# Kernel optimization log

Measured on AMD Instinct MI355X. Metric: run time of the kernel, lower is better.

The kernel has to match this reference:

```python
import jax, jax.numpy as jnp
import numpy as np

N = 100000
IN_C = 256
OUT_C = 256
E = 500000


def gcn_conv(x, W, b, edges):
    """PyG GCNConv: add self-loops, symmetric D^-1/2 (A+I) D^-1/2 normalization,
    then scatter-add of transformed source features into targets, plus bias."""
    n = x.shape[0]
    loop = jnp.arange(n, dtype=edges.dtype)
    row = jnp.concatenate([edges[0], loop])  # source
    col = jnp.concatenate([edges[1], loop])  # target
    deg = jax.ops.segment_sum(jnp.ones_like(col, dtype=x.dtype), col, num_segments=n)
    dis = jax.lax.rsqrt(deg)  # deg >= 1 after self-loops
    norm = dis[row] * dis[col]  # [E+n]
    h = x @ W  # [n, out]
    msg = h[row] * norm[:, None]  # gather + scale
    return jax.ops.segment_sum(msg, col, num_segments=n) + b


def setup_inputs() -> dict:
    key = jax.random.key(0)
    ks = jax.random.split(key, 24)
    x = jax.random.normal(ks[0], (N, IN_C), dtype=jnp.float32)
    edges00 = jax.random.randint(ks[1], (2, E), 0, N, dtype=jnp.int32)
    edges01 = jax.random.randint(ks[2], (2, E), 0, N, dtype=jnp.int32)
    edges10 = jax.random.randint(ks[3], (2, E), 0, N, dtype=jnp.int32)
    edges11 = jax.random.randint(ks[4], (2, E), 0, N, dtype=jnp.int32)
    t0 = (jax.random.uniform(ks[5], (N,)) > 0.5).astype(jnp.float32)
    t1 = 1.0 - t0
    scale = 1.0 / np.sqrt(IN_C)
    W1 = jax.random.normal(ks[6], (IN_C, OUT_C), dtype=jnp.float32) * scale
    W2 = jax.random.normal(ks[7], (IN_C, OUT_C), dtype=jnp.float32) * scale
    W3 = jax.random.normal(ks[8], (IN_C, OUT_C), dtype=jnp.float32) * scale
    W4 = jax.random.normal(ks[9], (IN_C, OUT_C), dtype=jnp.float32) * scale
    b1 = jnp.zeros((OUT_C,), jnp.float32)
    b2 = jnp.zeros((OUT_C,), jnp.float32)
    b3 = jnp.zeros((OUT_C,), jnp.float32)
    b4 = jnp.zeros((OUT_C,), jnp.float32)
    p0 = jax.random.normal(ks[10], (OUT_C,), dtype=jnp.float32)
    p1 = jax.random.normal(ks[11], (OUT_C,), dtype=jnp.float32)
    p2 = jax.random.normal(ks[12], (OUT_C,), dtype=jnp.float32)
    p3 = jax.random.normal(ks[13], (OUT_C,), dtype=jnp.float32)
    p4 = jax.random.normal(ks[14], (OUT_C,), dtype=jnp.float32)
    p5 = jax.random.normal(ks[15], (OUT_C,), dtype=jnp.float32)
    return dict(x=x, edges00=edges00, edges01=edges01, edges10=edges10, edges11=edges11,
                type0_idx=t0, type1_idx=t1,
                W1=W1, b1=b1, W2=W2, b2=b2, W3=W3, b3=b3, W4=W4, b4=b4,
                p0=p0, p1=p1, p2=p2, p3=p3, p4=p4, p5=p5)


def reference(x, edges00, edges01, edges10, edges11, type0_idx, type1_idx,
              W1, b1, W2, b2, W3, b3, W4, b4, p0, p1, p2, p3, p4, p5):
    # x0/x1: first feature column masked by node type, broadcast over out channels
    x0c = type0_idx * x[:, 0]  # [N]
    x1c = type1_idx * x[:, 0]
    x00 = gcn_conv(x, W1, b1, edges00)
    x01 = gcn_conv(x, W2, b2, edges01)
    x10 = gcn_conv(x, W3, b3, edges10)
    x11 = gcn_conv(x, W4, b4, edges11)
    out = (x0c[:, None] * p0 + x1c[:, None] * p1
           + x00 * p2 + x01 * p3 + x10 * p4 + x11 * p5)
    return out
```

## Files before the change

kernel.cpp:

```cpp
#include <hip/hip_runtime.h>


typedef __bf16 v8bf __attribute__((ext_vector_type(8)));
typedef float v4f __attribute__((ext_vector_type(4)));

__device__ __forceinline__ unsigned short f2bf(float f) {
  unsigned u = __float_as_uint(f);
  u += 0x7fffu + ((u >> 16) & 1u);
  return (unsigned short)(u >> 16);
}
__device__ __forceinline__ float bf2f(unsigned short s) {
  return __uint_as_float(((unsigned)s) << 16);
}
__device__ __forceinline__ void async_ld16(const void* g, void* l) {
  __builtin_amdgcn_global_load_lds((__attribute__((address_space(1))) void*)g,
                                   (__attribute__((address_space(3))) void*)l,
                                   16, 0, 0);
}

__global__ void lc_zero(int* __restrict__ p, int n) {
  int i = blockIdx.x * 256 + threadIdx.x;
  if (i < n) p[i] = 0;
}

__global__ void lc_hist(const int* __restrict__ e0, const int* __restrict__ e1,
                        const int* __restrict__ e2, const int* __restrict__ e3,
                        int* __restrict__ hist, int N, int E) {
  int e = blockIdx.x * 256 + threadIdx.x;
  if (e >= E) return;
  int k = blockIdx.y;
  const int* ed = (k == 0) ? e0 : (k == 1) ? e1 : (k == 2) ? e2 : e3;
  int col = ed[E + e];
  atomicAdd(&hist[k * N + col], 1);
}

__global__ void lc_dis(const int* __restrict__ hist, float* __restrict__ dis, int M) {
  int i = blockIdx.x * 256 + threadIdx.x;
  if (i < M) dis[i] = rsqrtf((float)(hist[i] + 1));
}

__global__ void lc_scan1(const int* __restrict__ in, int* __restrict__ outp,
                         int* __restrict__ bsum, int M) {
  __shared__ int tmp[256];
  int t = threadIdx.x, i = blockIdx.x * 256 + t;
  int v = (i < M) ? in[i] : 0;
  tmp[t] = v;
  __syncthreads();
  for (int off = 1; off < 256; off <<= 1) {
    int add = (t >= off) ? tmp[t - off] : 0;
    __syncthreads();
    tmp[t] += add;
    __syncthreads();
  }
  if (i < M) outp[i] = tmp[t] - v;
  if (t == 255) bsum[blockIdx.x] = tmp[255];
}

__global__ void lc_scan2(int* __restrict__ bsum, int nb) {
  __shared__ int tmp[256];
  __shared__ int carry_s;
  int t = threadIdx.x;
  if (t == 0) carry_s = 0;
  __syncthreads();
  for (int base = 0; base < nb; base += 256) {
    int i = base + t;
    int v = (i < nb) ? bsum[i] : 0;
    tmp[t] = v;
    __syncthreads();
    for (int off = 1; off < 256; off <<= 1) {
      int add = (t >= off) ? tmp[t - off] : 0;
      __syncthreads();
      tmp[t] += add;
      __syncthreads();
    }
    int carry = carry_s;
    int total = tmp[255];
    if (i < nb) bsum[i] = carry + tmp[t] - v;
    __syncthreads();
    if (t == 0) carry_s = carry + total;
    __syncthreads();
  }
}

__global__ void lc_scan3(int* __restrict__ rp, int* __restrict__ cursor,
                         const int* __restrict__ bsum, int M) {
  int i = blockIdx.x * 256 + threadIdx.x;
  if (i < M) {
    int v = rp[i] + bsum[blockIdx.x];
    rp[i] = v;
    cursor[i] = v;
  }
}

__global__ void lc_fill(const int* __restrict__ e0, const int* __restrict__ e1,
                        const int* __restrict__ e2, const int* __restrict__ e3,
                        int* __restrict__ cursor, const float* __restrict__ dis,
                        int2* __restrict__ payload, int N, int E) {
  int e = blockIdx.x * 256 + threadIdx.x;
  if (e >= E) return;
  int k = blockIdx.y;
  const int* ed = (k == 0) ? e0 : (k == 1) ? e1 : (k == 2) ? e2 : e3;
  int src = ed[e], col = ed[E + e];
  int pos = atomicAdd(&cursor[k * N + col], 1);
  float nrm = dis[k * N + src] * dis[k * N + col];
  payload[pos] = make_int2(src, __float_as_int(nrm));
}

__global__ void lc_bias(const float* __restrict__ b1, const float* __restrict__ b2,
                        const float* __restrict__ b3, const float* __restrict__ b4,
                        const float* __restrict__ p2, const float* __restrict__ p3,
                        const float* __restrict__ p4, const float* __restrict__ p5,
                        float* __restrict__ biasc) {
  int c = threadIdx.x;
  biasc[c] = b1[c] * p2[c] + b2[c] * p3[c] + b3[c] * p4[c] + b4[c] * p5[c];
}

__global__ void lc_prep(const float* __restrict__ W1, const float* __restrict__ W2,
                        const float* __restrict__ W3, const float* __restrict__ W4,
                        const float* __restrict__ p2, const float* __restrict__ p3,
                        const float* __restrict__ p4, const float* __restrict__ p5,
                        unsigned short* __restrict__ Wt) {
  int b = blockIdx.x;
  int k = b >> 8, co = b & 255;
  int kk = threadIdx.x;
  const float* W = (k == 0) ? W1 : (k == 1) ? W2 : (k == 2) ? W3 : W4;
  const float* p = (k == 0) ? p2 : (k == 1) ? p3 : (k == 2) ? p4 : p5;
  Wt[(size_t)co * 1024 + k * 256 + kk] = f2bf(W[kk * 256 + co] * p[co]);
}

__global__ void lc_cvt(const float4* __restrict__ x4, ushort4* __restrict__ xb4,
                       const float* __restrict__ t0, const float* __restrict__ t1,
                       float* __restrict__ m0, float* __restrict__ m1, int n4) {
  int i = blockIdx.x * 256 + threadIdx.x;
  if (i >= n4) return;
  float4 v = x4[i];
  ushort4 r;
  r.x = f2bf(v.x); r.y = f2bf(v.y); r.z = f2bf(v.z); r.w = f2bf(v.w);
  xb4[i] = r;
  if ((i & 63) == 0) {
    int n = i >> 6;
    float xc = v.x;
    m0[n] = t0[n] * xc;
    m1[n] = t1[n] * xc;
  }
}

__global__ __launch_bounds__(256) void lc_aggx(
    const unsigned short* __restrict__ xb, unsigned short* __restrict__ Agg,
    int aggw, int kcount, int kbase, const int* __restrict__ rp,
    const int* __restrict__ hist, const float* __restrict__ dis,
    const int2* __restrict__ payload, int N) {
  int t = threadIdx.x;
  int w = t >> 6, lane = t & 63;
  int n, k, koff;
  if (kcount == 4) { n = blockIdx.x; k = w; koff = k * 256; }
  else { n = blockIdx.x * 4 + w; k = kbase; koff = 0; }
  if (n >= N) return;
  int c = lane * 4;
  int idx = k * N + n;

  float dn = dis[idx];
  float s = dn * dn;
  ushort4 hv = *(const ushort4*)&xb[(size_t)n * 256 + c];
  float a0 = bf2f(hv.x) * s, a1 = bf2f(hv.y) * s;
  float a2 = bf2f(hv.z) * s, a3 = bf2f(hv.w) * s;

  int start = rp[idx];
  int cnt = hist[idx];
  int i = 0;
  for (; i + 4 <= cnt; i += 4) {
    int2 e0 = payload[start + i];
    int2 e1 = payload[start + i + 1];
    int2 e2 = payload[start + i + 2];
    int2 e3 = payload[start + i + 3];
    ushort4 g0 = *(const ushort4*)&xb[(size_t)e0.x * 256 + c];
    ushort4 g1 = *(const ushort4*)&xb[(size_t)e1.x * 256 + c];
    ushort4 g2 = *(const ushort4*)&xb[(size_t)e2.x * 256 + c];
    ushort4 g3 = *(const ushort4*)&xb[(size_t)e3.x * 256 + c];
    float n0 = __int_as_float(e0.y), n1 = __int_as_float(e1.y);
    float n2 = __int_as_float(e2.y), n3 = __int_as_float(e3.y);
    a0 += bf2f(g0.x) * n0 + bf2f(g1.x) * n1 + bf2f(g2.x) * n2 + bf2f(g3.x) * n3;
    a1 += bf2f(g0.y) * n0 + bf2f(g1.y) * n1 + bf2f(g2.y) * n2 + bf2f(g3.y) * n3;
    a2 += bf2f(g0.z) * n0 + bf2f(g1.z) * n1 + bf2f(g2.z) * n2 + bf2f(g3.z) * n3;
    a3 += bf2f(g0.w) * n0 + bf2f(g1.w) * n1 + bf2f(g2.w) * n2 + bf2f(g3.w) * n3;
  }
  for (; i < cnt; i++) {
    int2 e0 = payload[start + i];
    ushort4 g0 = *(const ushort4*)&xb[(size_t)e0.x * 256 + c];
    float n0 = __int_as_float(e0.y);
    a0 += bf2f(g0.x) * n0;
    a1 += bf2f(g0.y) * n0;
    a2 += bf2f(g0.z) * n0;
    a3 += bf2f(g0.w) * n0;
  }
  ushort4 r;
  r.x = f2bf(a0); r.y = f2bf(a1); r.z = f2bf(a2); r.w = f2bf(a3);
  *(ushort4*)&Agg[(size_t)n * aggw + koff + c] = r;
}

__global__ __launch_bounds__(256) void lc_gemm(
    const unsigned short* __restrict__ A, int strideA,
    const unsigned short* __restrict__ B, int strideB, int K,
    float* __restrict__ out, int Mrows, int addprev, int doepi,
    const float* __restrict__ m0, const float* __restrict__ m1,
    const float* __restrict__ p0, const float* __restrict__ p1,
    const float* __restrict__ biasc) {
  __shared__ alignas(16) unsigned short As[128 * 32];
  __shared__ alignas(16) unsigned short Bs[128 * 32];
  int t = threadIdx.x;
  int w = t >> 6, lane = t & 63;
  int wm = w & 1, wn = w >> 1;
  int quad = lane >> 4, l16 = lane & 15;
  int row0 = blockIdx.x * 128, col0 = blockIdx.y * 128;

  v4f acc[4][4];
#pragma unroll
  for (int mt = 0; mt < 4; mt++)
#pragma unroll
    for (int nt = 0; nt < 4; nt++) {
      v4f z = {0.f, 0.f, 0.f, 0.f};
      acc[mt][nt] = z;
    }

  for (int kk = 0; kk < K; kk += 32) {
#pragma unroll
    for (int p = 0; p < 2; p++) {
      int cbase = p * 256 + w * 64;
      int cA = cbase + lane;
      int rl = cA >> 2, c16 = cA & 3;
      int grow = row0 + rl;
      if (grow >= Mrows) grow = Mrows - 1;
      async_ld16(A + (size_t)grow * strideA + kk + c16 * 8, &As[cbase * 8]);
      async_ld16(B + (size_t)(col0 + rl) * strideB + kk + c16 * 8, &Bs[cbase * 8]);
    }
    __syncthreads();

    v8bf af[4], bfr[4];
#pragma unroll
    for (int mt = 0; mt < 4; mt++) {
      int r = wm * 64 + mt * 16 + l16;
      af[mt] = *(const v8bf*)&As[r * 32 + quad * 8];
    }
#pragma unroll
    for (int nt = 0; nt < 4; nt++) {
      int n = wn * 64 + nt * 16 + l16;
      bfr[nt] = *(const v8bf*)&Bs[n * 32 + quad * 8];
    }
#pragma unroll
    for (int mt = 0; mt < 4; mt++)
#pragma unroll
      for (int nt = 0; nt < 4; nt++)
        acc[mt][nt] =
            __builtin_amdgcn_mfma_f32_16x16x32_bf16(af[mt], bfr[nt], acc[mt][nt], 0, 0, 0);
    __syncthreads();
  }

  float pc0[4], pc1[4], bc[4];
#pragma unroll
  for (int nt = 0; nt < 4; nt++) {
    int gcol = col0 + wn * 64 + nt * 16 + l16;
    pc0[nt] = doepi ? p0[gcol] : 0.f;
    pc1[nt] = doepi ? p1[gcol] : 0.f;
    bc[nt] = doepi ? biasc[gcol] : 0.f;
  }
#pragma unroll
  for (int mt = 0; mt < 4; mt++)
#pragma unroll
    for (int r = 0; r < 4; r++) {
      int grow = row0 + wm * 64 + mt * 16 + quad * 4 + r;
      if (grow >= Mrows) continue;
      float m0v = 0.f, m1v = 0.f;
      if (doepi) { m0v = m0[grow]; m1v = m1[grow]; }
#pragma unroll
      for (int nt = 0; nt < 4; nt++) {
        int gcol = col0 + wn * 64 + nt * 16 + l16;
        size_t o = (size_t)grow * 256 + gcol;
        float v = acc[mt][nt][r];
        if (addprev) v += out[o];
        if (doepi) v += m0v * pc0[nt] + m1v * pc1[nt] + bc[nt];
        out[o] = v;
      }
    }
}

extern "C" void kernel_launch(void* const* d_in, const int* in_sizes, int n_in,
                              void* d_out, int out_size, void* d_ws, size_t ws_size,
                              hipStream_t stream) {
  const float* x = (const float*)d_in[0];
  const int* e00 = (const int*)d_in[1];
  const int* e01 = (const int*)d_in[2];
  const int* e10 = (const int*)d_in[3];
  const int* e11 = (const int*)d_in[4];
  const float* t0 = (const float*)d_in[5];
  const float* t1 = (const float*)d_in[6];
  const float* W1 = (const float*)d_in[7];
  const float* b1 = (const float*)d_in[8];
  const float* W2 = (const float*)d_in[9];
  const float* b2 = (const float*)d_in[10];
  const float* W3 = (const float*)d_in[11];
  const float* b3 = (const float*)d_in[12];
  const float* W4 = (const float*)d_in[13];
  const float* b4 = (const float*)d_in[14];
  const float* p0 = (const float*)d_in[15];
  const float* p1 = (const float*)d_in[16];
  const float* p2 = (const float*)d_in[17];
  const float* p3 = (const float*)d_in[18];
  const float* p4 = (const float*)d_in[19];
  const float* p5 = (const float*)d_in[20];
  float* out = (float*)d_out;

  int N = in_sizes[0] / 256;
  int E = in_sizes[1] / 2;
  int M4 = 4 * N;
  int nb = (M4 + 255) / 256;

  char* wp = (char*)d_ws;
  auto carve = [&](size_t bytes) {
    void* r = (void*)wp;
    wp += (bytes + 255) & ~(size_t)255;
    return r;
  };
  unsigned short* xb = (unsigned short*)carve((size_t)N * 256 * 2);
  unsigned short* Wt = (unsigned short*)carve((size_t)256 * 1024 * 2);
  int* hist = (int*)carve((size_t)M4 * 4);
  float* dis = (float*)carve((size_t)M4 * 4);
  int* rp = (int*)carve((size_t)M4 * 4);
  int* cursor = (int*)carve((size_t)M4 * 4);
  int* bsum = (int*)carve((size_t)nb * 4);
  float* biasc = (float*)carve(256 * 4);
  float* m0 = (float*)carve((size_t)N * 4);
  float* m1 = (float*)carve((size_t)N * 4);
  int2* payload = (int2*)carve((size_t)4 * E * 8);
  size_t used = (size_t)(wp - (char*)d_ws);
  size_t remain = (ws_size > used) ? ws_size - used : 0;
  bool fat = remain >= (size_t)N * 1024 * 2;
  unsigned short* Agg = (unsigned short*)wp;

  int gE = (E + 255) / 256;
  int gM = (M4 + 255) / 256;

  lc_zero<<<gM, 256, 0, stream>>>(hist, M4);
  lc_hist<<<dim3(gE, 4), 256, 0, stream>>>(e00, e01, e10, e11, hist, N, E);
  lc_dis<<<gM, 256, 0, stream>>>(hist, dis, M4);
  lc_scan1<<<nb, 256, 0, stream>>>(hist, rp, bsum, M4);
  lc_scan2<<<1, 256, 0, stream>>>(bsum, nb);
  lc_scan3<<<nb, 256, 0, stream>>>(rp, cursor, bsum, M4);
  lc_fill<<<dim3(gE, 4), 256, 0, stream>>>(e00, e01, e10, e11, cursor, dis, payload, N, E);
  lc_bias<<<1, 256, 0, stream>>>(b1, b2, b3, b4, p2, p3, p4, p5, biasc);
  lc_prep<<<1024, 256, 0, stream>>>(W1, W2, W3, W4, p2, p3, p4, p5, Wt);
  lc_cvt<<<(N * 64 + 255) / 256, 256, 0, stream>>>((const float4*)x, (ushort4*)xb,
                                                   t0, t1, m0, m1, N * 64);

  int gemm_mb = (N + 127) / 128;
  if (fat) {
    lc_aggx<<<N, 256, 0, stream>>>(xb, Agg, 1024, 4, 0, rp, hist, dis, payload, N);
    lc_gemm<<<dim3(gemm_mb, 2), 256, 0, stream>>>(Agg, 1024, Wt, 1024, 1024, out, N,
                                                  0, 1, m0, m1, p0, p1, biasc);
  } else {
    for (int k = 0; k < 4; k++) {
      lc_aggx<<<(N + 3) / 4, 256, 0, stream>>>(xb, Agg, 256, 1, k, rp, hist, dis,
                                               payload, N);
      lc_gemm<<<dim3(gemm_mb, 2), 256, 0, stream>>>(Agg, 256, Wt + k * 256, 1024, 256,
                                                    out, N, (k > 0) ? 1 : 0,
                                                    (k == 3) ? 1 : 0, m0, m1, p0, p1,
                                                    biasc);
    }
  }
}
```

Baseline: 721.5 us.

## Fuse neighbor aggregation and GEMM into one kernel with aggregated rows kept in LDS

Replaces the separate aggregation kernel, which wrote a bf16 Agg buffer to global memory, and the tiled GEMM with one fused kernel. Each 512-thread block aggregates 32 nodes across all four edge types into a swizzled LDS tile, then runs MFMA directly against W read from global memory, and applies the epilogue. Two edge types are gathered at once per wave to raise memory-level parallelism. This removes the round trip of the intermediate through HBM and the extra launches. The trade-offs are 64KB of LDS per block and B operands read from global or cache with no LDS staging.

```diff
diff --git a/kernel.cpp b/kernel.cpp
--- a/kernel.cpp
+++ b/kernel.cpp
@@ -11,11 +11,6 @@
 }
 __device__ __forceinline__ float bf2f(unsigned short s) {
   return __uint_as_float(((unsigned)s) << 16);
-}
-__device__ __forceinline__ void async_ld16(const void* g, void* l) {
-  __builtin_amdgcn_global_load_lds((__attribute__((address_space(1))) void*)g,
-                                   (__attribute__((address_space(3))) void*)l,
-                                   16, 0, 0);
 }
 
 __global__ void lc_zero(int* __restrict__ p, int n) {
@@ -145,140 +140,128 @@
   }
 }
 
-__global__ __launch_bounds__(256) void lc_aggx(
-    const unsigned short* __restrict__ xb, unsigned short* __restrict__ Agg,
-    int aggw, int kcount, int kbase, const int* __restrict__ rp,
-    const int* __restrict__ hist, const float* __restrict__ dis,
-    const int2* __restrict__ payload, int N) {
-  int t = threadIdx.x;
-  int w = t >> 6, lane = t & 63;
-  int n, k, koff;
-  if (kcount == 4) { n = blockIdx.x; k = w; koff = k * 256; }
-  else { n = blockIdx.x * 4 + w; k = kbase; koff = 0; }
-  if (n >= N) return;
-  int c = lane * 4;
-  int idx = k * N + n;
-
-  float dn = dis[idx];
-  float s = dn * dn;
-  ushort4 hv = *(const ushort4*)&xb[(size_t)n * 256 + c];
-  float a0 = bf2f(hv.x) * s, a1 = bf2f(hv.y) * s;
-  float a2 = bf2f(hv.z) * s, a3 = bf2f(hv.w) * s;
-
-  int start = rp[idx];
-  int cnt = hist[idx];
-  int i = 0;
-  for (; i + 4 <= cnt; i += 4) {
-    int2 e0 = payload[start + i];
-    int2 e1 = payload[start + i + 1];
-    int2 e2 = payload[start + i + 2];
-    int2 e3 = payload[start + i + 3];
-    ushort4 g0 = *(const ushort4*)&xb[(size_t)e0.x * 256 + c];
-    ushort4 g1 = *(const ushort4*)&xb[(size_t)e1.x * 256 + c];
-    ushort4 g2 = *(const ushort4*)&xb[(size_t)e2.x * 256 + c];
-    ushort4 g3 = *(const ushort4*)&xb[(size_t)e3.x * 256 + c];
-    float n0 = __int_as_float(e0.y), n1 = __int_as_float(e1.y);
-    float n2 = __int_as_float(e2.y), n3 = __int_as_float(e3.y);
-    a0 += bf2f(g0.x) * n0 + bf2f(g1.x) * n1 + bf2f(g2.x) * n2 + bf2f(g3.x) * n3;
-    a1 += bf2f(g0.y) * n0 + bf2f(g1.y) * n1 + bf2f(g2.y) * n2 + bf2f(g3.y) * n3;
-    a2 += bf2f(g0.z) * n0 + bf2f(g1.z) * n1 + bf2f(g2.z) * n2 + bf2f(g3.z) * n3;
-    a3 += bf2f(g0.w) * n0 + bf2f(g1.w) * n1 + bf2f(g2.w) * n2 + bf2f(g3.w) * n3;
-  }
-  for (; i < cnt; i++) {
-    int2 e0 = payload[start + i];
-    ushort4 g0 = *(const ushort4*)&xb[(size_t)e0.x * 256 + c];
-    float n0 = __int_as_float(e0.y);
-    a0 += bf2f(g0.x) * n0;
-    a1 += bf2f(g0.y) * n0;
-    a2 += bf2f(g0.z) * n0;
-    a3 += bf2f(g0.w) * n0;
-  }
-  ushort4 r;
-  r.x = f2bf(a0); r.y = f2bf(a1); r.z = f2bf(a2); r.w = f2bf(a3);
-  *(ushort4*)&Agg[(size_t)n * aggw + koff + c] = r;
-}
-
-__global__ __launch_bounds__(256) void lc_gemm(
-    const unsigned short* __restrict__ A, int strideA,
-    const unsigned short* __restrict__ B, int strideB, int K,
-    float* __restrict__ out, int Mrows, int addprev, int doepi,
+#define GAT1(POS, A0, A1, A2, A3)                                       \
+  do {                                                                  \
+    int2 ee = payload[POS];                                             \
+    ushort4 gg = *(const ushort4*)&xb[(size_t)ee.x * 256 + c];          \
+    float nn = __int_as_float(ee.y);                                    \
+    A0 += bf2f(gg.x) * nn;                                              \
+    A1 += bf2f(gg.y) * nn;                                              \
+    A2 += bf2f(gg.z) * nn;                                              \
+    A3 += bf2f(gg.w) * nn;                                              \
+  } while (0)
+
+__global__ __launch_bounds__(512, 4) void lc_fused(
+    const unsigned short* __restrict__ xb, const unsigned short* __restrict__ Wt,
+    const int* __restrict__ rp, const int* __restrict__ hist,
+    const float* __restrict__ dis, const int2* __restrict__ payload,
+    float* __restrict__ out, int N,
     const float* __restrict__ m0, const float* __restrict__ m1,
     const float* __restrict__ p0, const float* __restrict__ p1,
     const float* __restrict__ biasc) {
-  __shared__ alignas(16) unsigned short As[128 * 32];
-  __shared__ alignas(16) unsigned short Bs[128 * 32];
-  int t = threadIdx.x;
-  int w = t >> 6, lane = t & 63;
-  int wm = w & 1, wn = w >> 1;
-  int quad = lane >> 4, l16 = lane & 15;
-  int row0 = blockIdx.x * 128, col0 = blockIdx.y * 128;
-
-  v4f acc[4][4];
-#pragma unroll
-  for (int mt = 0; mt < 4; mt++)
-#pragma unroll
-    for (int nt = 0; nt < 4; nt++) {
+  __shared__ alignas(16) unsigned short As[32 * 1024];
+  const int t = threadIdx.x;
+  const int w = t >> 6, lane = t & 63;
+  const int quad = lane >> 4, l16 = lane & 15;
+  const int n0 = blockIdx.x * 32;
+  const int c = lane * 4;
+
+  for (int pb = 0; pb < 16; pb += 2) {
+    int pr = w * 16 + pb;
+    int ln = pr >> 2;
+    int k0 = pr & 3;
+    int n = n0 + ln;
+    if (n >= N) n = N - 1;
+    int idx0 = k0 * N + n;
+    int idx1 = idx0 + N;
+    float d0 = dis[idx0], d1 = dis[idx1];
+    float s0v = d0 * d0, s1v = d1 * d1;
+    ushort4 hv = *(const ushort4*)&xb[(size_t)n * 256 + c];
+    float x0 = bf2f(hv.x), x1 = bf2f(hv.y), x2 = bf2f(hv.z), x3 = bf2f(hv.w);
+    float a0 = x0 * s0v, a1 = x1 * s0v, a2 = x2 * s0v, a3 = x3 * s0v;
+    float b0 = x0 * s1v, b1 = x1 * s1v, b2 = x2 * s1v, b3 = x3 * s1v;
+    int st0 = rp[idx0], cnt0 = hist[idx0];
+    int st1 = rp[idx1], cnt1 = hist[idx1];
+    int i0 = 0, i1 = 0;
+    while (i0 + 4 <= cnt0 && i1 + 4 <= cnt1) {
+      GAT1(st0 + i0 + 0, a0, a1, a2, a3);
+      GAT1(st0 + i0 + 1, a0, a1, a2, a3);
+      GAT1(st0 + i0 + 2, a0, a1, a2, a3);
+      GAT1(st0 + i0 + 3, a0, a1, a2, a3);
+      GAT1(st1 + i1 + 0, b0, b1, b2, b3);
+      GAT1(st1 + i1 + 1, b0, b1, b2, b3);
+      GAT1(st1 + i1 + 2, b0, b1, b2, b3);
+      GAT1(st1 + i1 + 3, b0, b1, b2, b3);
+      i0 += 4;
+      i1 += 4;
+    }
+    for (; i0 + 4 <= cnt0; i0 += 4) {
+      GAT1(st0 + i0 + 0, a0, a1, a2, a3);
+      GAT1(st0 + i0 + 1, a0, a1, a2, a3);
+      GAT1(st0 + i0 + 2, a0, a1, a2, a3);
+      GAT1(st0 + i0 + 3, a0, a1, a2, a3);
+    }
+    for (; i0 < cnt0; ++i0) GAT1(st0 + i0, a0, a1, a2, a3);
+    for (; i1 + 4 <= cnt1; i1 += 4) {
+      GAT1(st1 + i1 + 0, b0, b1, b2, b3);
+      GAT1(st1 + i1 + 1, b0, b1, b2, b3);
+      GAT1(st1 + i1 + 2, b0, b1, b2, b3);
+      GAT1(st1 + i1 + 3, b0, b1, b2, b3);
+    }
+    for (; i1 < cnt1; ++i1) GAT1(st1 + i1, b0, b1, b2, b3);
+
+    unsigned swz = (unsigned)((ln & 7) << 3);
+    ushort4 r0, r1;
+    r0.x = f2bf(a0); r0.y = f2bf(a1); r0.z = f2bf(a2); r0.w = f2bf(a3);
+    r1.x = f2bf(b0); r1.y = f2bf(b1); r1.z = f2bf(b2); r1.w = f2bf(b3);
+    *(ushort4*)&As[(unsigned)ln * 1024 + (((unsigned)(k0 * 256 + c)) ^ swz)] = r0;
+    *(ushort4*)&As[(unsigned)ln * 1024 + (((unsigned)((k0 + 1) * 256 + c)) ^ swz)] = r1;
+  }
+  __syncthreads();
+
+  v4f acc[2][2];
+#pragma unroll
+  for (int mt = 0; mt < 2; mt++)
+#pragma unroll
+    for (int nt = 0; nt < 2; nt++) {
       v4f z = {0.f, 0.f, 0.f, 0.f};
       acc[mt][nt] = z;
     }
 
-  for (int kk = 0; kk < K; kk += 32) {
-#pragma unroll
-    for (int p = 0; p < 2; p++) {
-      int cbase = p * 256 + w * 64;
-      int cA = cbase + lane;
-      int rl = cA >> 2, c16 = cA & 3;
-      int grow = row0 + rl;
-      if (grow >= Mrows) grow = Mrows - 1;
-      async_ld16(A + (size_t)grow * strideA + kk + c16 * 8, &As[cbase * 8]);
-      async_ld16(B + (size_t)(col0 + rl) * strideB + kk + c16 * 8, &Bs[cbase * 8]);
-    }
-    __syncthreads();
-
-    v8bf af[4], bfr[4];
-#pragma unroll
-    for (int mt = 0; mt < 4; mt++) {
-      int r = wm * 64 + mt * 16 + l16;
-      af[mt] = *(const v8bf*)&As[r * 32 + quad * 8];
-    }
-#pragma unroll
-    for (int nt = 0; nt < 4; nt++) {
-      int n = wn * 64 + nt * 16 + l16;
-      bfr[nt] = *(const v8bf*)&Bs[n * 32 + quad * 8];
-    }
-#pragma unroll
-    for (int mt = 0; mt < 4; mt++)
-#pragma unroll
-      for (int nt = 0; nt < 4; nt++)
-        acc[mt][nt] =
-            __builtin_amdgcn_mfma_f32_16x16x32_bf16(af[mt], bfr[nt], acc[mt][nt], 0, 0, 0);
-    __syncthreads();
-  }
-
-  float pc0[4], pc1[4], bc[4];
-#pragma unroll
-  for (int nt = 0; nt < 4; nt++) {
-    int gcol = col0 + wn * 64 + nt * 16 + l16;
-    pc0[nt] = doepi ? p0[gcol] : 0.f;
-    pc1[nt] = doepi ? p1[gcol] : 0.f;
-    bc[nt] = doepi ? biasc[gcol] : 0.f;
-  }
-#pragma unroll
-  for (int mt = 0; mt < 4; mt++)
+  const unsigned short* Bp = Wt + (size_t)(w * 32 + l16) * 1024 + quad * 8;
+#pragma unroll 4
+  for (int kk = 0; kk < 1024; kk += 32) {
+    int eq = (kk + quad * 8) ^ ((l16 & 7) << 3);
+    v8bf af0 = *(const v8bf*)&As[(unsigned)l16 * 1024 + eq];
+    v8bf af1 = *(const v8bf*)&As[(unsigned)(l16 + 16) * 1024 + eq];
+    v8bf bq0 = *(const v8bf*)&Bp[kk];
+    v8bf bq1 = *(const v8bf*)&Bp[16384 + kk];
+    acc[0][0] = __builtin_amdgcn_mfma_f32_16x16x32_bf16(af0, bq0, acc[0][0], 0, 0, 0);
+    acc[0][1] = __builtin_amdgcn_mfma_f32_16x16x32_bf16(af0, bq1, acc[0][1], 0, 0, 0);
+    acc[1][0] = __builtin_amdgcn_mfma_f32_16x16x32_bf16(af1, bq0, acc[1][0], 0, 0, 0);
+    acc[1][1] = __builtin_amdgcn_mfma_f32_16x16x32_bf16(af1, bq1, acc[1][1], 0, 0, 0);
+  }
+
+  float pc0[2], pc1[2], bcv[2];
+#pragma unroll
+  for (int nt = 0; nt < 2; nt++) {
+    int gcol = w * 32 + nt * 16 + l16;
+    pc0[nt] = p0[gcol];
+    pc1[nt] = p1[gcol];
+    bcv[nt] = biasc[gcol];
+  }
+#pragma unroll
+  for (int mt = 0; mt < 2; mt++)
 #pragma unroll
     for (int r = 0; r < 4; r++) {
-      int grow = row0 + wm * 64 + mt * 16 + quad * 4 + r;
-      if (grow >= Mrows) continue;
-      float m0v = 0.f, m1v = 0.f;
-      if (doepi) { m0v = m0[grow]; m1v = m1[grow]; }
-#pragma unroll
-      for (int nt = 0; nt < 4; nt++) {
-        int gcol = col0 + wn * 64 + nt * 16 + l16;
-        size_t o = (size_t)grow * 256 + gcol;
-        float v = acc[mt][nt][r];
-        if (addprev) v += out[o];
-        if (doepi) v += m0v * pc0[nt] + m1v * pc1[nt] + bc[nt];
-        out[o] = v;
+      int grow = n0 + mt * 16 + quad * 4 + r;
+      if (grow >= N) continue;
+      float m0v = m0[grow], m1v = m1[grow];
+#pragma unroll
+      for (int nt = 0; nt < 2; nt++) {
+        int gcol = w * 32 + nt * 16 + l16;
+        out[(size_t)grow * 256 + gcol] =
+            acc[mt][nt][r] + m0v * pc0[nt] + m1v * pc1[nt] + bcv[nt];
       }
     }
 }
@@ -331,10 +314,6 @@
   float* m0 = (float*)carve((size_t)N * 4);
   float* m1 = (float*)carve((size_t)N * 4);
   int2* payload = (int2*)carve((size_t)4 * E * 8);
-  size_t used = (size_t)(wp - (char*)d_ws);
-  size_t remain = (ws_size > used) ? ws_size - used : 0;
-  bool fat = remain >= (size_t)N * 1024 * 2;
-  unsigned short* Agg = (unsigned short*)wp;
 
   int gE = (E + 255) / 256;
   int gM = (M4 + 255) / 256;
@@ -351,19 +330,6 @@
   lc_cvt<<<(N * 64 + 255) / 256, 256, 0, stream>>>((const float4*)x, (ushort4*)xb,
                                                    t0, t1, m0, m1, N * 64);
 
-  int gemm_mb = (N + 127) / 128;
-  if (fat) {
-    lc_aggx<<<N, 256, 0, stream>>>(xb, Agg, 1024, 4, 0, rp, hist, dis, payload, N);
-    lc_gemm<<<dim3(gemm_mb, 2), 256, 0, stream>>>(Agg, 1024, Wt, 1024, 1024, out, N,
-                                                  0, 1, m0, m1, p0, p1, biasc);
-  } else {
-    for (int k = 0; k < 4; k++) {
-      lc_aggx<<<(N + 3) / 4, 256, 0, stream>>>(xb, Agg, 256, 1, k, rp, hist, dis,
-                                               payload, N);
-      lc_gemm<<<dim3(gemm_mb, 2), 256, 0, stream>>>(Agg, 256, Wt + k * 256, 1024, 256,
-                                                    out, N, (k > 0) ? 1 : 0,
-                                                    (k == 3) ? 1 : 0, m0, m1, p0, p1,
-                                                    biasc);
-    }
-  }
-}
+  lc_fused<<<dim3((N + 31) / 32), 512, 0, stream>>>(xb, Wt, rp, hist, dis, payload,
+                                                    out, N, m0, m1, p0, p1, biasc);
+}
```

After: 821.3 us. 1.14x slower.
